# Optimization experiments

Measured on AMD Instinct MI355X. Metric: run time of the kernel, lower is better.

## Reference

```python
import jax, jax.numpy as jnp
import numpy as np


def setup_inputs() -> dict:
    N, E, F, M, D = 50000, 200000, 64, 64, 128
    L = 3
    LAMBS = jnp.array([1.0, 0.1, 0.01], jnp.float32) * 12.0  # lambs * output
    R = int(np.ceil(np.sqrt(N)))  # n_virtuals = 224
    RAW = M * L + F  # raw_message_dimension = 256
    key = jax.random.key(0)
    ks = jax.random.split(key, 16)

    def lin(k, i, o):
        return jax.random.normal(k, (i, o), jnp.float32) / np.float32(np.sqrt(i))

    return dict(
        source_nodes=jax.random.randint(ks[0], (E,), 0, N),
        target_nodes=jax.random.randint(ks[1], (E,), 0, N),
        timestamps=jax.random.uniform(ks[2], (E,), jnp.float32),
        now_time=jnp.ones((1,), jnp.float32),
        predict_IND=0,
        node_features=0.1 * jax.random.normal(ks[3], (N, F), jnp.float32),
        memory=jnp.concatenate([0.05 * jax.random.normal(ks[4], (N, L, M), jnp.float32), jnp.ones((N, L, 1), jnp.float32)], axis=-1),
        last_update=jnp.zeros((N,), jnp.float32),
        virtual_memory=0.05 * jax.random.normal(ks[5], (R, L, M), jnp.float32),
        virtual_last_update=jnp.zeros((R,), jnp.float32),
        A_r=jnp.ones((N, R), jnp.float32) + jax.random.uniform(ks[6], (N, R), jnp.float32) / 10.0,
        static_emb=0.1 * jax.random.normal(ks[7], (N, D), jnp.float32),
        lamb=jnp.array([0.5], jnp.float32),
        lambs=LAMBS,
        mf_W1=lin(ks[8], RAW, RAW // 2), mf_b1=jnp.zeros((RAW // 2,), jnp.float32),
        mf_W2=lin(ks[9], RAW // 2, M), mf_b2=jnp.zeros((M,), jnp.float32),
        ffr_W1=lin(ks[10], RAW, RAW), ffr_b1=jnp.zeros((RAW,), jnp.float32),
        ffr_W2=lin(ks[11], RAW, M), ffr_b2=jnp.zeros((M,), jnp.float32),
        et_W=lin(ks[12], L * M, M), et_b=jnp.zeros((M,), jnp.float32),
        st_W=lin(ks[13], 2 * M, D), st_b=jnp.zeros((D,), jnp.float32),
    )


def reference(source_nodes, target_nodes, timestamps, now_time, predict_IND,
              node_features, memory, last_update, virtual_memory, virtual_last_update,
              A_r, static_emb, lamb, lambs,
              mf_W1, mf_b1, mf_W2, mf_b2, ffr_W1, ffr_b1, ffr_W2, ffr_b2,
              et_W, et_b, st_W, st_b):
    N, L, Mp1 = memory.shape
    M = Mp1 - 1
    R = virtual_memory.shape[0]
    E = source_nodes.shape[0]
    eps = 1e-6

    # exp_lambs embedding of targets: memory ratio [E, L*M]
    mem_t = memory[target_nodes]
    tgt_emb = (mem_t[:, :, :-1] / mem_t[:, :, -1:]).reshape(E, L * M)
    # raw message = [target_embedding, node_features[target], 1]  -> [E, RAW+1]
    src_msg = jnp.concatenate([tgt_emb, node_features[target_nodes], jnp.ones((E, 1), tgt_emb.dtype)], axis=1)

    # exp_lambs aggregation: decay every event to the latest timestamp of its source node
    t_max = jax.ops.segment_max(timestamps, source_nodes, num_segments=N)
    cnt = jax.ops.segment_sum(jnp.ones((E,), timestamps.dtype), source_nodes, num_segments=N)
    has_msg = cnt > 0
    t_max = jnp.where(has_msg, t_max, 0.0)
    w = jnp.exp(-lambs[None, :] * (t_max[source_nodes][:, None] - timestamps[:, None]))  # [E, L]
    agg = jax.ops.segment_sum(w[:, :, None] * src_msg[:, None, :], source_nodes, num_segments=N)  # [N, L, RAW+1]

    # MLP message function on feature channels, carry the weight-count channel along
    feat = agg[:, :, :-1]  # [N, L, RAW]
    h = jax.nn.relu(feat @ mf_W1 + mf_b1)
    msg_feat = jax.nn.relu(h @ mf_W2 + mf_b2)  # [N, L, M]
    messages = jnp.concatenate([msg_feat, agg[:, :, -1:]], axis=-1)  # [N, L, M+1]

    # virtual-node routing: A = softmax(A_r, axis=0) restricted to active nodes
    A = jax.nn.softmax(A_r, axis=0) * has_msg[:, None].astype(A_r.dtype)  # [N, R]
    B = jnp.where(has_msg[:, None, None], feat / jnp.maximum(agg[:, :, -1:], eps), 0.0)  # [N, L, RAW]
    vmid = jnp.einsum('nr,nlf->rlf', A, B)  # [R, L, RAW]
    vh = jax.nn.leaky_relu(vmid @ ffr_W1 + ffr_b1)
    vmsg = jax.nn.leaky_relu(vh @ ffr_W2 + ffr_b2)  # [R, L, M]

    # node memory exp-decay update (only active nodes)
    dt = jnp.where(has_msg, t_max - last_update, 0.0)
    decay = jnp.exp(-lambs[None, :, None] * dt[:, None, None])  # [N, L, 1]
    new_mem = jnp.where(has_msg[:, None, None], memory * decay + messages, memory)
    node_emb = (new_mem[:, :, :-1] / jnp.maximum(new_mem[:, :, -1:], eps)).reshape(N, L * M)

    # virtual memory exp-decay update to now_time
    vdt = now_time[0] - virtual_last_update  # [R]
    vdecay = jnp.exp(-lambs[None, :] * vdt[:, None])  # [R, L]
    new_vmem = virtual_memory * vdecay[:, :, None] + vmsg
    v_emb = new_vmem.reshape(R, L * M)

    r2n = jax.nn.softmax(A_r, axis=1)  # [N, R]
    vnode_emb = r2n @ v_emb  # [N, L*M]

    dyn = jnp.concatenate([node_emb, vnode_emb], axis=0)  # [2N, L*M]
    hh = jax.nn.leaky_relu(dyn @ et_W + et_b)  # [2N, M]
    hh = hh.reshape(2, N, M).transpose(1, 0, 2).reshape(N, 2 * M)
    spat = jax.nn.leaky_relu(hh @ st_W + st_b)  # [N, D]
    return lamb[0] * static_emb + (1.0 - lamb[0]) * spat
```

## Files before the change

kernel.cpp:

```cpp
#include <hip/hip_runtime.h>

static __device__ __forceinline__ float lky(float x) { return x > 0.f ? x : 0.01f * x; }

static __device__ __forceinline__ unsigned short f2bf(float x) {
    unsigned int u = __float_as_uint(x);
    unsigned int r = (u + 0x7FFFu + ((u >> 16) & 1u)) >> 16;
    return (unsigned short)r;
}
static __device__ __forceinline__ float bf2f(unsigned short x) {
    return __uint_as_float((unsigned int)x << 16);
}
static __device__ __forceinline__ unsigned int pack2bf(float lo, float hi) {
    return (unsigned int)f2bf(lo) | ((unsigned int)f2bf(hi) << 16);
}

typedef __attribute__((ext_vector_type(8))) short short8;
typedef __attribute__((ext_vector_type(4))) float f32x4;

constexpr int SN  = 50048;
constexpr int KLV = 1216;
constexpr int VCM = 42;

__global__ void k_init(float* t_max, int* cnt, int* cursor, float* colsum, int N) {
    int i = blockIdx.x * 256 + threadIdx.x;
    if (i < N) { t_max[i] = -1.0f; cnt[i] = 0; cursor[i] = 0; }
    if (i < 224) colsum[i] = 0.0f;
}

__global__ void k_tbf(const float* __restrict__ src, unsigned short* __restrict__ dst,
                      int K, int C) {
    int i = blockIdx.x * 256 + threadIdx.x;
    if (i >= K * C) return;
    int c = i / K, k = i % K;
    dst[i] = f2bf(src[k * C + c]);
}

__global__ void k_tmax_cnt(const int* __restrict__ src, const float* __restrict__ ts,
                           float* t_max, int* cnt, int E) {
    int e = blockIdx.x * 256 + threadIdx.x;
    if (e >= E) return;
    int s = src[e];
    atomicMax((int*)(t_max + s), __float_as_int(ts[e]));
    atomicAdd(cnt + s, 1);
}

__global__ __launch_bounds__(1024) void k_scan(const int* __restrict__ cnt,
                                               int* __restrict__ offsets, int N) {
    __shared__ int wsum[16];
    __shared__ int s_run;
    int t = threadIdx.x;
    int lane = t & 63, wid = t >> 6;
    if (t == 0) s_run = 0;
    __syncthreads();
    int nchunk = (N + 1023) >> 10;
    for (int c = 0; c < nchunk; ++c) {
        int i = (c << 10) + t;
        int v = (i < N) ? cnt[i] : 0;
        int x = v;
        #pragma unroll
        for (int d = 1; d < 64; d <<= 1) {
            int y = __shfl_up(x, d, 64);
            if (lane >= d) x += y;
        }
        if (lane == 63) wsum[wid] = x;
        __syncthreads();
        int wbase = 0;
        #pragma unroll
        for (int w = 0; w < 16; ++w) wbase += (w < wid) ? wsum[w] : 0;
        int run = s_run;
        if (i < N) offsets[i] = run + wbase + x - v;
        __syncthreads();
        if (t == 1023) s_run = run + wbase + x;
        __syncthreads();
    }
    if (t == 0) offsets[N] = s_run;
}

__global__ void k_scatter(const int* __restrict__ src, const int* __restrict__ offsets,
                          int* cursor, int* sorted, int E) {
    int e = blockIdx.x * 256 + threadIdx.x;
    if (e >= E) return;
    int s = src[e];
    int pos = offsets[s] + atomicAdd(cursor + s, 1);
    sorted[pos] = e;
}

__global__ __launch_bounds__(256) void k_prep(
        const float* __restrict__ memory, const float* __restrict__ nodef,
        unsigned int* __restrict__ temb, int N) {
    int wid = threadIdx.x >> 6, lane = threadIdx.x & 63;
    int n = blockIdx.x * 4 + wid;
    if (n >= N) return;
    const float* mrow = memory + (size_t)n * 195;
    float d0 = mrow[64], d1 = mrow[129], d2 = mrow[194];
    int f = 2 * lane;
    float den = (f < 64) ? d0 : d1;
    int offA = (f < 64) ? f : f + 1;
    float va0 = mrow[offA] / den;
    float va1 = mrow[offA + 1] / den;
    float vb0, vb1;
    if (lane < 32) {
        vb0 = mrow[130 + 2 * lane] / d2;
        vb1 = mrow[131 + 2 * lane] / d2;
    } else {
        const float* nf = nodef + (size_t)n * 64 + 2 * (lane - 32);
        vb0 = nf[0]; vb1 = nf[1];
    }
    temb[(size_t)n * 128 + lane]      = pack2bf(va0, va1);
    temb[(size_t)n * 128 + 64 + lane] = pack2bf(vb0, vb1);
}

__global__ __launch_bounds__(256) void k_aexp(
        const float* __restrict__ A_r,
        float* __restrict__ rowsum, float* __restrict__ colsum,
        unsigned short* __restrict__ AexpT, unsigned short* __restrict__ Aexp_rm, int N) {
    __shared__ unsigned short sE[64][226];
    int t = threadIdx.x, lane = t & 63, w = t >> 6;
    int n0 = blockIdx.x * 64;
    for (int i = 0; i < 16; ++i) {
        int n = w * 16 + i;
        int gn = n0 + n;
        float e0 = 0.f, e1 = 0.f, e2 = 0.f, e3 = 0.f;
        if (gn < N) {
            const float* row = A_r + (size_t)gn * 224;
            e0 = __expf(row[lane]);
            e1 = __expf(row[64 + lane]);
            e2 = __expf(row[128 + lane]);
            if (lane < 32) e3 = __expf(row[192 + lane]);
        }
        sE[n][lane]       = f2bf(e0);
        sE[n][64 + lane]  = f2bf(e1);
        sE[n][128 + lane] = f2bf(e2);
        if (lane < 32) sE[n][192 + lane] = f2bf(e3);
        float rs = e0 + e1 + e2 + e3;
        #pragma unroll
        for (int d = 32; d > 0; d >>= 1) rs += __shfl_xor(rs, d, 64);
        if (lane == 0 && gn < N) rowsum[gn] = rs;
    }
    __syncthreads();
    if (t < 224) {
        float s = 0.f;
        #pragma unroll 8
        for (int r = 0; r < 64; ++r) s += bf2f(sE[r][t]);
        atomicAdd(colsum + t, s);
    }
    {
        unsigned int* dst = (unsigned int*)Aexp_rm;
        for (int i = t; i < 64 * 112; i += 256) {
            int n = i / 112, cp = i % 112;
            unsigned int v = *(const unsigned int*)&sE[n][2 * cp];
            dst[(size_t)(n0 + n) * 112 + cp] = v;
        }
    }
    {
        unsigned int* dst = (unsigned int*)AexpT;
        for (int u = t; u < 224 * 32; u += 256) {
            int r = u >> 5, np = u & 31;
            unsigned int lo = sE[2 * np][r];
            unsigned int hi = sE[2 * np + 1][r];
            dst[(size_t)r * (SN / 2) + (n0 >> 1) + np] = lo | (hi << 16);
        }
    }
}

__global__ __launch_bounds__(256) void k_agg(
        const int* __restrict__ tgt, const float* __restrict__ ts,
        const int* __restrict__ sorted, const int* __restrict__ offsets,
        const float* __restrict__ t_max, const unsigned int* __restrict__ temb,
        const float* __restrict__ lambs,
        unsigned int* __restrict__ aggb, float* __restrict__ cnt3,
        int* __restrict__ has_msg, int N) {
    int wid = threadIdx.x >> 6, lane = threadIdx.x & 63;
    int n = blockIdx.x * 4 + wid;
    size_t rb = (size_t)n * 3;
    if (n >= N) {
        #pragma unroll
        for (int l = 0; l < 3; ++l) {
            unsigned int* row = aggb + (rb + l) * 128;
            row[lane] = 0; row[64 + lane] = 0;
            if (lane == 0) cnt3[rb + l] = 0.f;
        }
        return;
    }
    int beg = offsets[n], end = offsets[n + 1];
    float lb0 = lambs[0], lb1 = lambs[1], lb2 = lambs[2];
    float tm = t_max[n];
    float aa0[3], aa1[3], ab0[3], ab1[3], accc[3];
    #pragma unroll
    for (int l = 0; l < 3; ++l) { aa0[l] = aa1[l] = ab0[l] = ab1[l] = accc[l] = 0.f; }
    for (int idx = beg; idx < end; ++idx) {
        int e = sorted[idx];
        int tt = tgt[e];
        float d = tm - ts[e];
        unsigned int ua = temb[(size_t)tt * 128 + lane];
        unsigned int ub = temb[(size_t)tt * 128 + 64 + lane];
        float a0 = __uint_as_float(ua << 16);
        float a1 = __uint_as_float(ua & 0xffff0000u);
        float b0 = __uint_as_float(ub << 16);
        float b1 = __uint_as_float(ub & 0xffff0000u);
        float w0 = __expf(-lb0 * d), w1 = __expf(-lb1 * d), w2 = __expf(-lb2 * d);
        aa0[0] += w0 * a0; aa1[0] += w0 * a1; ab0[0] += w0 * b0; ab1[0] += w0 * b1; accc[0] += w0;
        aa0[1] += w1 * a0; aa1[1] += w1 * a1; ab0[1] += w1 * b0; ab1[1] += w1 * b1; accc[1] += w1;
        aa0[2] += w2 * a0; aa1[2] += w2 * a1; ab0[2] += w2 * b0; ab1[2] += w2 * b1; accc[2] += w2;
    }
    #pragma unroll
    for (int l = 0; l < 3; ++l) {
        unsigned int* row = aggb + (rb + l) * 128;
        row[lane]      = pack2bf(aa0[l], aa1[l]);
        row[64 + lane] = pack2bf(ab0[l], ab1[l]);
        if (lane == 0) cnt3[rb + l] = accc[l];
    }
    if (lane == 0) has_msg[n] = (end > beg) ? 1 : 0;
}

__global__ __launch_bounds__(256) void k_mf_mfma(
        const unsigned short* __restrict__ aggb,
        const unsigned short* __restrict__ W1T, const float* __restrict__ b1,
        const unsigned short* __restrict__ W2T, const float* __restrict__ b2,
        unsigned short* __restrict__ msg_feat, int NROWS) {
    __shared__ unsigned short As[64 * 264];
    __shared__ unsigned short Hs[64 * 136];
    int t = threadIdx.x, lane = t & 63, w = t >> 6;
    int lr = lane & 15, kg = lane >> 4;
    int row0 = blockIdx.x * 64;
    {
        int r = t >> 2, s4 = t & 3;
        const uint4* src = (const uint4*)(aggb + (size_t)(row0 + r) * 256 + s4 * 64);
        uint4* dst = (uint4*)(As + r * 264 + s4 * 64);
        #pragma unroll
        for (int u = 0; u < 8; ++u) dst[u] = src[u];
    }
    __syncthreads();
    int n0 = w * 32;
    f32x4 acc[4][2];
    #pragma unroll
    for (int m = 0; m < 4; ++m) {
        acc[m][0] = (f32x4){0.f, 0.f, 0.f, 0.f};
        acc[m][1] = (f32x4){0.f, 0.f, 0.f, 0.f};
    }
    for (int kk = 0; kk < 8; ++kk) {
        short8 bf0 = *(const short8*)(W1T + (size_t)(n0 + lr) * 256 + kk * 32 + kg * 8);
        short8 bf1 = *(const short8*)(W1T + (size_t)(n0 + 16 + lr) * 256 + kk * 32 + kg * 8);
        #pragma unroll
        for (int m = 0; m < 4; ++m) {
            short8 af = *(const short8*)(As + (m * 16 + lr) * 264 + kk * 32 + kg * 8);
            acc[m][0] = __builtin_amdgcn_mfma_f32_16x16x32_bf16(af, bf0, acc[m][0], 0, 0, 0);
            acc[m][1] = __builtin_amdgcn_mfma_f32_16x16x32_bf16(af, bf1, acc[m][1], 0, 0, 0);
        }
    }
    float bb0 = b1[n0 + lr], bb1 = b1[n0 + 16 + lr];
    #pragma unroll
    for (int m = 0; m < 4; ++m)
        #pragma unroll
        for (int j = 0; j < 4; ++j) {
            int row = m * 16 + kg * 4 + j;
            Hs[row * 136 + n0 + lr]      = f2bf(fmaxf(acc[m][0][j] + bb0, 0.f));
            Hs[row * 136 + n0 + 16 + lr] = f2bf(fmaxf(acc[m][1][j] + bb1, 0.f));
        }
    __syncthreads();
    int c0 = w * 16;
    f32x4 a2[4];
    #pragma unroll
    for (int m = 0; m < 4; ++m) a2[m] = (f32x4){0.f, 0.f, 0.f, 0.f};
    for (int kk = 0; kk < 4; ++kk) {
        short8 bf = *(const short8*)(W2T + (size_t)(c0 + lr) * 128 + kk * 32 + kg * 8);
        #pragma unroll
        for (int m = 0; m < 4; ++m) {
            short8 af = *(const short8*)(Hs + (m * 16 + lr) * 136 + kk * 32 + kg * 8);
            a2[m] = __builtin_amdgcn_mfma_f32_16x16x32_bf16(af, bf, a2[m], 0, 0, 0);
        }
    }
    float b2v = b2[c0 + lr];
    #pragma unroll
    for (int m = 0; m < 4; ++m)
        #pragma unroll
        for (int j = 0; j < 4; ++j) {
            int row = row0 + m * 16 + kg * 4 + j;
            if (row < NROWS)
                msg_feat[(size_t)row * 64 + c0 + lr] = f2bf(fmaxf(a2[m][j] + b2v, 0.f));
        }
}

__global__ __launch_bounds__(256) void k_vmid_mfma(
        const unsigned short* __restrict__ AexpT, const unsigned short* __restrict__ aggb,
        const float* __restrict__ cnt3, float* __restrict__ vpart) {
    __shared__ unsigned short As[112 * 40];
    __shared__ float sDinv[32];
    int bx = blockIdx.x;
    int chunk = bx / 12, tile = bx % 12;
    int r0 = (tile & 1) * 112;
    int ft = tile >> 1;
    int l = ft >> 1, fo = (ft & 1) * 128;
    int t = threadIdx.x, lane = t & 63, w = t >> 6;
    int lr = lane & 15, kg = lane >> 4;
    f32x4 acc[7][2];
    #pragma unroll
    for (int q = 0; q < 7; ++q) {
        acc[q][0] = (f32x4){0.f, 0.f, 0.f, 0.f};
        acc[q][1] = (f32x4){0.f, 0.f, 0.f, 0.f};
    }
    int nbeg = chunk * KLV;
    int nsteps = min(KLV, SN - nbeg) >> 5;
    int colbase = fo + w * 32 + lr;
    for (int s = 0; s < nsteps; ++s) {
        int n0 = nbeg + s * 32;
        if (t < 224) {
            int srow = t >> 1, sseg = t & 1;
            const uint4* ap = (const uint4*)(AexpT + (size_t)(r0 + srow) * SN + n0) + sseg * 2;
            uint4 v0 = ap[0];
            uint4 v1 = ap[1];
            *(uint4*)&As[srow * 40 + sseg * 16]     = v0;
            *(uint4*)&As[srow * 40 + sseg * 16 + 8] = v1;
        } else {
            int k = t - 224;
            sDinv[k] = 1.f / fmaxf(cnt3[(size_t)(n0 + k) * 3 + l], 1e-6f);
        }
        __syncthreads();
        short8 b0, b1;
        #pragma unroll
        for (int j = 0; j < 8; ++j) {
            int kk = kg * 8 + j;
            float dv = sDinv[kk];
            const unsigned short* brow = aggb + ((size_t)(n0 + kk) * 3 + l) * 256 + colbase;
            b0[j] = (short)f2bf(bf2f(brow[0])  * dv);
            b1[j] = (short)f2bf(bf2f(brow[16]) * dv);
        }
        #pragma unroll
        for (int q = 0; q < 7; ++q) {
            short8 af = *(const short8*)&As[(q * 16 + lr) * 40 + kg * 8];
            acc[q][0] = __builtin_amdgcn_mfma_f32_16x16x32_bf16(af, b0, acc[q][0], 0, 0, 0);
            acc[q][1] = __builtin_amdgcn_mfma_f32_16x16x32_bf16(af, b1, acc[q][1], 0, 0, 0);
        }
        __syncthreads();
    }
    float* outp = vpart + (size_t)chunk * 172032;
    #pragma unroll
    for (int q = 0; q < 7; ++q) {
        int row = r0 + q * 16 + kg * 4;
        #pragma unroll
        for (int p = 0; p < 2; ++p) {
            int col = l * 256 + fo + w * 32 + p * 16 + lr;
            #pragma unroll
            for (int j = 0; j < 4; ++j)
                outp[(size_t)(row + j) * 768 + col] = acc[q][p][j];
        }
    }
}

__global__ void k_vred(const float* __restrict__ vpart, const float* __restrict__ colsum,
                       float* __restrict__ vmid) {
    int idx = blockIdx.x * 256 + threadIdx.x;
    if (idx >= 224 * 768) return;
    float s = 0.f;
    for (int c = 0; c < VCM; ++c) s += vpart[(long)c * (224 * 768) + idx];
    vmid[idx] = s / colsum[idx / 768];
}

__global__ __launch_bounds__(256) void k_ffr(
        const float* __restrict__ vmid, const float* __restrict__ W1, const float* __restrict__ b1,
        const float* __restrict__ W2, const float* __restrict__ b2,
        const float* __restrict__ vmem, const float* __restrict__ vlast,
        const float* __restrict__ lambs, const float* __restrict__ now_time,
        unsigned short* __restrict__ vembT) {
    __shared__ float sin_[16][260];
    __shared__ float svh[16][260];
    int row0 = blockIdx.x * 16;
    int t = threadIdx.x;
    #pragma unroll
    for (int k = 0; k < 16; ++k) {
        int idx = t + k * 256;
        int r = idx >> 8, f = idx & 255;
        sin_[r][f] = vmid[(long)(row0 + r) * 256 + f];
    }
    __syncthreads();
    {
        int cg = t & 63, rg = t >> 6;
        int c0 = cg * 4, r0 = rg * 4;
        float acc[4][4];
        #pragma unroll
        for (int i = 0; i < 4; ++i)
            #pragma unroll
            for (int j = 0; j < 4; ++j) acc[i][j] = 0.f;
        for (int f0 = 0; f0 < 256; f0 += 4) {
            float4 a[4];
            #pragma unroll
            for (int i = 0; i < 4; ++i) a[i] = *(const float4*)&sin_[r0 + i][f0];
            #pragma unroll
            for (int ff = 0; ff < 4; ++ff) {
                float4 w = *(const float4*)&W1[(long)(f0 + ff) * 256 + c0];
                #pragma unroll
                for (int i = 0; i < 4; ++i) {
                    float av = (&a[i].x)[ff];
                    acc[i][0] += av * w.x; acc[i][1] += av * w.y;
                    acc[i][2] += av * w.z; acc[i][3] += av * w.w;
                }
            }
        }
        #pragma unroll
        for (int i = 0; i < 4; ++i)
            #pragma unroll
            for (int j = 0; j < 4; ++j)
                svh[r0 + i][c0 + j] = lky(acc[i][j] + b1[c0 + j]);
    }
    __syncthreads();
    {
        int cg = t & 31, rg = t >> 5;
        int c0 = cg * 2, r0 = rg * 2;
        float acc[2][2];
        acc[0][0] = acc[0][1] = acc[1][0] = acc[1][1] = 0.f;
        for (int f0 = 0; f0 < 256; f0 += 4) {
            float4 a[2];
            #pragma unroll
            for (int i = 0; i < 2; ++i) a[i] = *(const float4*)&svh[r0 + i][f0];
            #pragma unroll
            for (int ff = 0; ff < 4; ++ff) {
                float2 w = *(const float2*)&W2[(long)(f0 + ff) * 64 + c0];
                #pragma unroll
                for (int i = 0; i < 2; ++i) {
                    float av = (&a[i].x)[ff];
                    acc[i][0] += av * w.x; acc[i][1] += av * w.y;
                }
            }
        }
        float nowv = now_time[0];
        #pragma unroll
        for (int i = 0; i < 2; ++i) {
            int row = row0 + r0 + i;
            int rr = row / 3, l = row % 3;
            float vd = __expf(-lambs[l] * (nowv - vlast[rr]));
            #pragma unroll
            for (int j = 0; j < 2; ++j) {
                float v = lky(acc[i][j] + b2[c0 + j]);
                int m = c0 + j;
                vembT[(size_t)(l * 64 + m) * 224 + rr] =
                    f2bf(vmem[(long)rr * 192 + l * 64 + m] * vd + v);
            }
        }
    }
}

__global__ void k_newmem(const float* __restrict__ memory,
        const unsigned short* __restrict__ msg_feat,
        const float* __restrict__ cnt3, const float* __restrict__ t_max,
        const float* __restrict__ last_update, const int* __restrict__ has_msg,
        const float* __restrict__ lambs, unsigned short* __restrict__ node_emb, int N) {
    int n = blockIdx.x;
    int j = threadIdx.x;
    int l = j >> 6, m = j & 63;
    int has = has_msg[n];
    float dt = has ? (t_max[n] - last_update[n]) : 0.f;
    float decay = __expf(-lambs[l] * dt);
    long mb = (long)n * 195 + l * 65;
    float num = memory[mb + m];
    float den = memory[mb + 64];
    if (has) {
        num = num * decay + bf2f(msg_feat[(size_t)n * 192 + j]);
        den = den * decay + cnt3[(size_t)n * 3 + l];
    }
    node_emb[(size_t)n * 192 + j] = f2bf(num / fmaxf(den, 1e-6f));
}

__global__ __launch_bounds__(256) void k_vnode_mfma(
        const unsigned short* __restrict__ Aexp_rm, const unsigned short* __restrict__ vembT,
        const float* __restrict__ rowsum, unsigned short* __restrict__ vnode_emb, int N) {
    __shared__ unsigned short As[64 * 232];
    __shared__ float sRS[64];
    int t = threadIdx.x, lane = t & 63, w = t >> 6;
    int lr = lane & 15, kg = lane >> 4;
    int row0 = blockIdx.x * 64;
    {
        int r = t >> 2, sg = t & 3;
        const uint4* src = (const uint4*)(Aexp_rm + (size_t)(row0 + r) * 224 + sg * 56);
        uint4* dst = (uint4*)(As + r * 232 + sg * 56);
        #pragma unroll
        for (int u = 0; u < 7; ++u) dst[u] = src[u];
    }
    if (t < 64) sRS[t] = rowsum[min(row0 + t, N - 1)];
    __syncthreads();
    int n0 = w * 48;
    f32x4 acc[4][3];
    #pragma unroll
    for (int m = 0; m < 4; ++m)
        #pragma unroll
        for (int nt = 0; nt < 3; ++nt) acc[m][nt] = (f32x4){0.f, 0.f, 0.f, 0.f};
    for (int kk = 0; kk < 7; ++kk) {
        short8 bf[3];
        #pragma unroll
        for (int nt = 0; nt < 3; ++nt)
            bf[nt] = *(const short8*)(vembT + (size_t)(n0 + nt * 16 + lr) * 224 + kk * 32 + kg * 8);
        #pragma unroll
        for (int m = 0; m < 4; ++m) {
            short8 af = *(const short8*)(As + (m * 16 + lr) * 232 + kk * 32 + kg * 8);
            #pragma unroll
            for (int nt = 0; nt < 3; ++nt)
                acc[m][nt] = __builtin_amdgcn_mfma_f32_16x16x32_bf16(af, bf[nt], acc[m][nt], 0, 0, 0);
        }
    }
    #pragma unroll
    for (int m = 0; m < 4; ++m)
        #pragma unroll
        for (int j = 0; j < 4; ++j) {
            int row = row0 + m * 16 + kg * 4 + j;
            if (row < N) {
                float inv = 1.f / sRS[row - row0];
                #pragma unroll
                for (int nt = 0; nt < 3; ++nt)
                    vnode_emb[(size_t)row * 192 + n0 + nt * 16 + lr] = f2bf(acc[m][nt][j] * inv);
            }
        }
}

__global__ __launch_bounds__(256) void k_et_st_mfma(
        const unsigned short* __restrict__ ne, const unsigned short* __restrict__ ve,
        const unsigned short* __restrict__ etWT, const float* __restrict__ etb,
        const unsigned short* __restrict__ stWT, const float* __restrict__ stb,
        const float* __restrict__ stat, const float* __restrict__ lamb,
        float* __restrict__ out, int N) {
    __shared__ unsigned short As[128 * 200];
    __shared__ unsigned short Hs[64 * 136];
    int t = threadIdx.x, lane = t & 63, w = t >> 6;
    int lr = lane & 15, kg = lane >> 4;
    int row0 = blockIdx.x * 64;
    {
        int r = t >> 2, sg = t & 3;
        const uint4* sn = (const uint4*)(ne + (size_t)(row0 + r) * 192 + sg * 48);
        const uint4* sv = (const uint4*)(ve + (size_t)(row0 + r) * 192 + sg * 48);
        uint4* dn = (uint4*)(As + (size_t)r * 200 + sg * 48);
        uint4* dv = (uint4*)(As + (size_t)(64 + r) * 200 + sg * 48);
        #pragma unroll
        for (int u = 0; u < 6; ++u) { dn[u] = sn[u]; dv[u] = sv[u]; }
    }
    __syncthreads();
    int c0 = w * 16;
    f32x4 acc[2][4];
    #pragma unroll
    for (int h = 0; h < 2; ++h)
        #pragma unroll
        for (int m = 0; m < 4; ++m) acc[h][m] = (f32x4){0.f, 0.f, 0.f, 0.f};
    for (int kk = 0; kk < 6; ++kk) {
        short8 bf = *(const short8*)(etWT + (size_t)(c0 + lr) * 192 + kk * 32 + kg * 8);
        #pragma unroll
        for (int h = 0; h < 2; ++h)
            #pragma unroll
            for (int m = 0; m < 4; ++m) {
                short8 af = *(const short8*)(As + (size_t)(h * 64 + m * 16 + lr) * 200 + kk * 32 + kg * 8);
                acc[h][m] = __builtin_amdgcn_mfma_f32_16x16x32_bf16(af, bf, acc[h][m], 0, 0, 0);
            }
    }
    float bb = etb[c0 + lr];
    #pragma unroll
    for (int h = 0; h < 2; ++h)
        #pragma unroll
        for (int m = 0; m < 4; ++m)
            #pragma unroll
            for (int j = 0; j < 4; ++j)
                Hs[(m * 16 + kg * 4 + j) * 136 + h * 64 + c0 + lr] = f2bf(lky(acc[h][m][j] + bb));
    __syncthreads();
    int c0s = w * 32;
    f32x4 a2[4][2];
    #pragma unroll
    for (int m = 0; m < 4; ++m) { a2[m][0] = (f32x4){0.f,0.f,0.f,0.f}; a2[m][1] = (f32x4){0.f,0.f,0.f,0.f}; }
    for (int kk = 0; kk < 4; ++kk) {
        short8 bf0 = *(const short8*)(stWT + (size_t)(c0s + lr) * 128 + kk * 32 + kg * 8);
        short8 bf1 = *(const short8*)(stWT + (size_t)(c0s + 16 + lr) * 128 + kk * 32 + kg * 8);
        #pragma unroll
        for (int m = 0; m < 4; ++m) {
            short8 af = *(const short8*)(Hs + (m * 16 + lr) * 136 + kk * 32 + kg * 8);
            a2[m][0] = __builtin_amdgcn_mfma_f32_16x16x32_bf16(af, bf0, a2[m][0], 0, 0, 0);
            a2[m][1] = __builtin_amdgcn_mfma_f32_16x16x32_bf16(af, bf1, a2[m][1], 0, 0, 0);
        }
    }
    float lam = lamb[0];
    float sb0 = stb[c0s + lr], sb1 = stb[c0s + 16 + lr];
    #pragma unroll
    for (int m = 0; m < 4; ++m)
        #pragma unroll
        for (int j = 0; j < 4; ++j) {
            int n = row0 + m * 16 + kg * 4 + j;
            if (n < N) {
                int ca = c0s + lr, cb = c0s + 16 + lr;
                float va = lky(a2[m][0][j] + sb0);
                float vb = lky(a2[m][1][j] + sb1);
                out[(size_t)n * 128 + ca] = lam * stat[(size_t)n * 128 + ca] + (1.f - lam) * va;
                out[(size_t)n * 128 + cb] = lam * stat[(size_t)n * 128 + cb] + (1.f - lam) * vb;
            }
        }
}

extern "C" void kernel_launch(void* const* d_in, const int* in_sizes, int n_in,
                              void* d_out, int out_size, void* d_ws, size_t ws_size,
                              hipStream_t stream) {
    const int*   src        = (const int*)d_in[0];
    const int*   tgt        = (const int*)d_in[1];
    const float* ts         = (const float*)d_in[2];
    const float* now_time   = (const float*)d_in[3];
    const float* nodef      = (const float*)d_in[5];
    const float* memory     = (const float*)d_in[6];
    const float* last_upd   = (const float*)d_in[7];
    const float* vmem       = (const float*)d_in[8];
    const float* vlast      = (const float*)d_in[9];
    const float* A_r        = (const float*)d_in[10];
    const float* static_emb = (const float*)d_in[11];
    const float* lamb       = (const float*)d_in[12];
    const float* lambs      = (const float*)d_in[13];
    const float* mf_W1      = (const float*)d_in[14];
    const float* mf_b1      = (const float*)d_in[15];
    const float* mf_W2      = (const float*)d_in[16];
    const float* mf_b2      = (const float*)d_in[17];
    const float* ffr_W1     = (const float*)d_in[18];
    const float* ffr_b1     = (const float*)d_in[19];
    const float* ffr_W2     = (const float*)d_in[20];
    const float* ffr_b2     = (const float*)d_in[21];
    const float* et_W       = (const float*)d_in[22];
    const float* et_b       = (const float*)d_in[23];
    const float* st_W       = (const float*)d_in[24];
    const float* st_b       = (const float*)d_in[25];

    int E = in_sizes[0];
    int N = in_sizes[7];

    float* ws = (float*)d_ws;
    size_t off = 0;
    auto alloc = [&](size_t nf) { float* p = ws + off; off += (nf + 63) & ~(size_t)63; return p; };
    unsigned short* aggb  = (unsigned short*)alloc((size_t)SN * 384);
    unsigned short* msg_feat = (unsigned short*)alloc((size_t)N * 96);
    unsigned short* AexpT   = (unsigned short*)alloc((size_t)224 * SN / 2);
    unsigned short* Aexp_rm = (unsigned short*)alloc((size_t)SN * 224 / 2);
    float* tv_union = alloc((size_t)VCM * 172032);
    float* vmid     = alloc(224 * 768);
    unsigned short* vembT = (unsigned short*)alloc((size_t)192 * 224 / 2 + 64);
    float* t_max    = alloc(N);
    float* rowsum   = alloc(N);
    float* cnt3     = alloc((size_t)SN * 3);
    float* colsum   = alloc(256);
    unsigned short* W1T  = (unsigned short*)alloc(128 * 256 / 2);
    unsigned short* W2T  = (unsigned short*)alloc(64 * 128 / 2);
    unsigned short* etWT = (unsigned short*)alloc(64 * 192 / 2);
    unsigned short* stWT = (unsigned short*)alloc(128 * 128 / 2);
    int*   cnt      = (int*)alloc(N);
    int*   offsets  = (int*)alloc(N + 1);
    int*   cursor   = (int*)alloc(N);
    int*   sorted   = (int*)alloc(E);
    int*   has_msg  = (int*)alloc(N);
    if (off * sizeof(float) > ws_size) return;

    unsigned int* temb = (unsigned int*)tv_union;
    float* vpart = tv_union;
    unsigned short* node_emb  = (unsigned short*)aggb;
    unsigned short* vnode_emb = node_emb + (size_t)N * 192;

    k_init<<<(N + 255) / 256, 256, 0, stream>>>(t_max, cnt, cursor, colsum, N);
    k_tbf<<<(256 * 128 + 255) / 256, 256, 0, stream>>>(mf_W1, W1T, 256, 128);
    k_tbf<<<(128 * 64 + 255) / 256, 256, 0, stream>>>(mf_W2, W2T, 128, 64);
    k_tbf<<<(192 * 64 + 255) / 256, 256, 0, stream>>>(et_W, etWT, 192, 64);
    k_tbf<<<(128 * 128 + 255) / 256, 256, 0, stream>>>(st_W, stWT, 128, 128);
    k_tmax_cnt<<<(E + 255) / 256, 256, 0, stream>>>(src, ts, t_max, cnt, E);
    k_scan<<<1, 1024, 0, stream>>>(cnt, offsets, N);
    k_scatter<<<(E + 255) / 256, 256, 0, stream>>>(src, offsets, cursor, sorted, E);
    k_prep<<<(N + 3) / 4, 256, 0, stream>>>(memory, nodef, temb, N);
    k_aexp<<<SN / 64, 256, 0, stream>>>(A_r, rowsum, colsum, AexpT, Aexp_rm, N);
    k_agg<<<SN / 4, 256, 0, stream>>>(tgt, ts, sorted, offsets, t_max, temb,
                                      lambs, (unsigned int*)aggb, cnt3, has_msg, N);
    k_mf_mfma<<<SN * 3 / 64, 256, 0, stream>>>(aggb, W1T, mf_b1, W2T, mf_b2, msg_feat, N * 3);
    k_vmid_mfma<<<12 * VCM, 256, 0, stream>>>(AexpT, aggb, cnt3, vpart);
    k_vred<<<(224 * 768 + 255) / 256, 256, 0, stream>>>(vpart, colsum, vmid);
    k_ffr<<<42, 256, 0, stream>>>(vmid, ffr_W1, ffr_b1, ffr_W2, ffr_b2, vmem, vlast,
                                  lambs, now_time, vembT);
    k_newmem<<<N, 192, 0, stream>>>(memory, msg_feat, cnt3, t_max, last_upd, has_msg,
                                    lambs, node_emb, N);
    k_vnode_mfma<<<SN / 64, 256, 0, stream>>>(Aexp_rm, vembT, rowsum, vnode_emb, N);
    k_et_st_mfma<<<SN / 64, 256, 0, stream>>>(node_emb, vnode_emb, etWT, et_b, stWT, st_b,
                                              static_emb, lamb, (float*)d_out, N);
}
```

Measured before the change: 431.0 us.

## Stage B operand through swizzled LDS transpose in vmid MFMA kernel

The vmid MFMA kernel used to gather the B operand with scalar 2-byte global loads per lane. It now loads it with coalesced 16-byte vector loads, scales each row by its inverse count, and writes it transposed into a bank-swizzled LDS tile, so each lane reads one short8 per operand. The K-chunk size is halved and the virtual chunk count roughly doubled to add parallelism. The cost is extra LDS traffic, more partial outputs to reduce, and a denser swizzle layout that must line up with the MFMA fragment indexing.

```diff
diff --git a/kernel.cpp b/kernel.cpp
--- a/kernel.cpp
+++ b/kernel.cpp
@@ -18,8 +18,8 @@
 typedef __attribute__((ext_vector_type(4))) float f32x4;
 
 constexpr int SN  = 50048;
-constexpr int KLV = 1216;
-constexpr int VCM = 42;
+constexpr int KLV = 608;
+constexpr int VCM = 83;
 
 __global__ void k_init(float* t_max, int* cnt, int* cursor, float* colsum, int N) {
     int i = blockIdx.x * 256 + threadIdx.x;
@@ -285,7 +285,7 @@
         const unsigned short* __restrict__ AexpT, const unsigned short* __restrict__ aggb,
         const float* __restrict__ cnt3, float* __restrict__ vpart) {
     __shared__ unsigned short As[112 * 40];
-    __shared__ float sDinv[32];
+    __shared__ unsigned int BsT[128 * 20];
     int bx = blockIdx.x;
     int chunk = bx / 12, tile = bx % 12;
     int r0 = (tile & 1) * 112;
@@ -293,6 +293,7 @@
     int l = ft >> 1, fo = (ft & 1) * 128;
     int t = threadIdx.x, lane = t & 63, w = t >> 6;
     int lr = lane & 15, kg = lane >> 4;
+    int np = t >> 4, sg = t & 15;
     f32x4 acc[7][2];
     #pragma unroll
     for (int q = 0; q < 7; ++q) {
@@ -301,7 +302,10 @@
     }
     int nbeg = chunk * KLV;
     int nsteps = min(KLV, SN - nbeg) >> 5;
-    int colbase = fo + w * 32 + lr;
+    int c0 = w * 32 + lr, c1 = c0 + 16;
+    int rb0 = c0 * 20 + (kg ^ ((c0 >> 3) & 3)) * 4;
+    int rb1 = c1 * 20 + (kg ^ ((c1 >> 3) & 3)) * 4;
+    int swz = np ^ ((sg & 3) << 2);
     for (int s = 0; s < nsteps; ++s) {
         int n0 = nbeg + s * 32;
         if (t < 224) {
@@ -311,20 +315,24 @@
             uint4 v1 = ap[1];
             *(uint4*)&As[srow * 40 + sseg * 16]     = v0;
             *(uint4*)&As[srow * 40 + sseg * 16 + 8] = v1;
-        } else {
-            int k = t - 224;
-            sDinv[k] = 1.f / fmaxf(cnt3[(size_t)(n0 + k) * 3 + l], 1e-6f);
+        }
+        {
+            int na = n0 + 2 * np;
+            size_t ra = ((size_t)na * 3 + l) * 256 + fo + sg * 8;
+            uint4 va = *(const uint4*)(aggb + ra);
+            uint4 vb = *(const uint4*)(aggb + ra + 768);
+            float da = 1.f / fmaxf(cnt3[(size_t)na * 3 + l], 1e-6f);
+            float db = 1.f / fmaxf(cnt3[(size_t)na * 3 + l + 3], 1e-6f);
+            const unsigned short* pa = (const unsigned short*)&va;
+            const unsigned short* pb = (const unsigned short*)&vb;
+            unsigned int* dst = BsT + sg * 160 + swz;
+            #pragma unroll
+            for (int j = 0; j < 8; ++j)
+                dst[j * 20] = pack2bf(bf2f(pa[j]) * da, bf2f(pb[j]) * db);
         }
         __syncthreads();
-        short8 b0, b1;
-        #pragma unroll
-        for (int j = 0; j < 8; ++j) {
-            int kk = kg * 8 + j;
-            float dv = sDinv[kk];
-            const unsigned short* brow = aggb + ((size_t)(n0 + kk) * 3 + l) * 256 + colbase;
-            b0[j] = (short)f2bf(bf2f(brow[0])  * dv);
-            b1[j] = (short)f2bf(bf2f(brow[16]) * dv);
-        }
+        short8 b0 = *(const short8*)((const unsigned short*)(BsT + rb0));
+        short8 b1 = *(const short8*)((const unsigned short*)(BsT + rb1));
         #pragma unroll
         for (int q = 0; q < 7; ++q) {
             short8 af = *(const short8*)&As[(q * 16 + lr) * 40 + kg * 8];
```

Result: no change. 425.1 us (-1.4%).
